# Kernel optimization log

Hardware: AMD Instinct MI355X
Metric: run time of the kernel (lower is better)

Reference implementation:

```python
import jax, jax.numpy as jnp
import numpy as np

N, E, DIN, DOUT = 50000, 625000, 128, 128


def setup_inputs() -> dict:
    key = jax.random.key(0)
    k = jax.random.split(key, 4)
    x = jax.random.normal(k[0], (N, DIN), dtype=jnp.float32)
    edge_index = jax.random.randint(k[1], (2, E), 0, N, dtype=jnp.int32)
    s = 1.0 / np.sqrt(DIN)  # Glorot-ish init like torch Linear
    W_fwd = jax.random.uniform(k[2], (DIN, DOUT), jnp.float32, -s, s)
    W_bwd = jax.random.uniform(k[3], (DIN, DOUT), jnp.float32, -s, s)
    b_fwd = jnp.zeros((DOUT,), jnp.float32)
    b_bwd = jnp.zeros((DOUT,), jnp.float32)
    return {"x": x, "edge_index": edge_index, "W_fwd": W_fwd, "b_fwd": b_fwd,
            "W_bwd": W_bwd, "b_bwd": b_bwd}


def gcn_conv(x, W, b, src, dst, n):
    """PyG GCNConv: add self-loops, symmetric degree norm, gather-scatter aggregate."""
    loops = jnp.arange(n, dtype=src.dtype)
    src2 = jnp.concatenate([src, loops])  # [E+N]
    dst2 = jnp.concatenate([dst, loops])
    ones = jnp.ones(src2.shape[0], dtype=x.dtype)
    deg = jax.ops.segment_sum(ones, dst2, num_segments=n)  # in-degree incl. self-loop
    dinv = jnp.where(deg > 0, jax.lax.rsqrt(deg), 0.0)
    norm = dinv[src2] * dinv[dst2]  # [E+N]
    h = x @ W  # [N, DOUT] dense GEMM before message passing
    msgs = h[src2] * norm[:, None]  # gather + scale, [E+N, DOUT]
    out = jax.ops.segment_sum(msgs, dst2, num_segments=n)  # scatter-add
    return out + b


def reference(x, edge_index, W_fwd, b_fwd, W_bwd, b_bwd):
    src, dst = edge_index[0], edge_index[1]
    n = x.shape[0]
    x_forward = gcn_conv(x, W_fwd, b_fwd, src, dst, n)
    # reversed edge direction for the backward diffusion conv
    x_backward = gcn_conv(x, W_bwd, b_bwd, dst, src, n)
    # dropout omitted (eval mode / deterministic reference)
    return jax.nn.relu(x_forward + x_backward)
```

## Files before the change

### kernel.cpp

```cpp
#include <hip/hip_runtime.h>
#include <hip/hip_bf16.h>
#include <cstdint>

static constexpr int BLK      = 256;
static constexpr int CAP      = 40;
static constexpr int BINSHIFT = 8;
static constexpr int BINNODES = 1 << BINSHIFT;
static constexpr int BINCAP   = BINNODES * CAP / 2;
static constexpr int EPB      = 2048;
static constexpr int OVMAX    = 1024;
static constexpr int NB2MAX   = 512;

typedef __attribute__((ext_vector_type(8))) short bf16x8;
typedef __attribute__((ext_vector_type(4))) float f32x4;

__device__ __forceinline__ float bf16lo(uint32_t u) { return __uint_as_float(u << 16); }
__device__ __forceinline__ float bf16hi(uint32_t u) { return __uint_as_float(u & 0xffff0000u); }
__device__ __forceinline__ float bf16f(unsigned short u) { return __uint_as_float((uint32_t)u << 16); }
__device__ __forceinline__ unsigned short f2bf(float f) {
    __hip_bfloat16 h = __float2bfloat16(f);
    return *(unsigned short*)&h;
}

__global__ __launch_bounds__(BLK) void k_bin_conv(
        const int* __restrict__ src, const int* __restrict__ dst, int ne,
        uint32_t* __restrict__ pair, int* __restrict__ gcnt,
        int* __restrict__ ovcnt, int* __restrict__ ovlist, int nbins, int gbin,
        const float* __restrict__ x, uint32_t* __restrict__ xb32, int nxw, int gxc,
        const float* __restrict__ Wf, const float* __restrict__ Wb,
        unsigned short* __restrict__ WTf, unsigned short* __restrict__ WTb) {
    const int bid = blockIdx.x, tid = threadIdx.x;
    if (bid < gbin) {
        __shared__ uint32_t stage[EPB * 2];
        __shared__ unsigned short binof[EPB * 2];
        __shared__ int hist[NB2MAX];
        __shared__ int lofs[NB2MAX];
        __shared__ int gbase[NB2MAX];
        __shared__ int chunk[NB2MAX / 8];
        const int nb2 = 2 * nbins;
        for (int i = tid; i < nb2; i += BLK) hist[i] = 0;
        __syncthreads();

        int s[8], d[8];
        const int e0 = bid * EPB + tid;
#pragma unroll
        for (int k = 0; k < 8; ++k) {
            int e = e0 + k * BLK;
            bool v = e < ne;
            s[k] = v ? src[e] : -1;
            d[k] = v ? dst[e] : -1;
            if (v) {
                atomicAdd(&hist[d[k] >> BINSHIFT], 1);
                atomicAdd(&hist[nbins + (s[k] >> BINSHIFT)], 1);
            }
        }
        __syncthreads();

        const int nch = (nb2 + 7) >> 3;
        if (tid < nch) {
            int a = 0, base = tid << 3;
#pragma unroll
            for (int k = 0; k < 8; ++k) { int idx = base + k; if (idx < nb2) a += hist[idx]; }
            chunk[tid] = a;
        }
        __syncthreads();
        if (tid == 0) { int a = 0; for (int c = 0; c < nch; ++c) { int t = chunk[c]; chunk[c] = a; a += t; } }
        __syncthreads();
        for (int i = tid; i < nb2; i += BLK) {
            int a = chunk[i >> 3];
            for (int k = (i >> 3) << 3; k < i; ++k) a += hist[k];
            lofs[i] = a;
        }
        __syncthreads();
        for (int i = tid; i < nb2; i += BLK) {
            int c = hist[i];
            gbase[i] = c ? atomicAdd(&gcnt[i], c) : 0;
            hist[i] = lofs[i];
        }
        __syncthreads();
#pragma unroll
        for (int k = 0; k < 8; ++k) {
            if (s[k] >= 0) {
                int b0 = d[k] >> BINSHIFT;
                int p0 = atomicAdd(&hist[b0], 1);
                stage[p0] = ((uint32_t)d[k] << 16) | (uint32_t)s[k];
                binof[p0] = (unsigned short)b0;
                int b1 = nbins + (s[k] >> BINSHIFT);
                int p1 = atomicAdd(&hist[b1], 1);
                stage[p1] = ((uint32_t)s[k] << 16) | (uint32_t)d[k];
                binof[p1] = (unsigned short)b1;
            }
        }
        __syncthreads();
        int nval = ne - bid * EPB; if (nval > EPB) nval = EPB; if (nval < 0) nval = 0;
        const int total = 2 * nval;
        for (int i = tid; i < total; i += BLK) {
            int b = binof[i];
            int gidx = gbase[b] + (i - lofs[b]);
            if (gidx < BINCAP)
                pair[(size_t)b * BINCAP + gidx] = stage[i];
            else {
                int node = (int)(stage[i] >> 16);
                int q = atomicAdd(ovcnt, 1);
                if (q < OVMAX) ovlist[q] = (node << 1) | (b >= nbins ? 1 : 0);
            }
        }
        return;
    }
    if (bid < gbin + gxc) {
        int base = (bid - gbin) * 2048;
        int end = base + 2048; if (end > nxw) end = nxw;
        for (int i = base + tid; i < end; i += BLK) {
            float2 v = ((const float2*)x)[i];
            xb32[i] = ((uint32_t)f2bf(v.y) << 16) | (uint32_t)f2bf(v.x);
        }
        return;
    }
    int wb = bid - gbin - gxc;
    for (int idx = wb * 2048 + tid; idx < (wb + 1) * 2048; idx += BLK) {
        int c = idx >> 7, k = idx & 127;
        WTf[c * 128 + k] = f2bf(Wf[k * 128 + c]);
        WTb[c * 128 + k] = f2bf(Wb[k * 128 + c]);
    }
}

__global__ __launch_bounds__(BLK) void k_build(
        uint32_t* __restrict__ pair, const int* __restrict__ gcnt,
        int* __restrict__ cnt_f, int* __restrict__ cnt_b,
        float* __restrict__ dinv_f, float* __restrict__ dinv_b,
        int* __restrict__ ovcnt, int* __restrict__ ovlist,
        int n, int nbins) {
    const int bid = blockIdx.x, tid = threadIdx.x;
    __shared__ unsigned short buck[BINNODES * CAP];
    __shared__ int lcnt[BINNODES];
    lcnt[tid] = 0;
    __syncthreads();
    int count = gcnt[bid]; if (count > BINCAP) count = BINCAP;
    const uint32_t* pb = pair + (size_t)bid * BINCAP;
    const int dir = bid >= nbins ? 1 : 0;
    for (int i = tid; i < count; i += BLK) {
        uint32_t p = pb[i];
        int l = (p >> 16) & (BINNODES - 1);
        int r = atomicAdd(&lcnt[l], 1);
        if (r < CAP) buck[l * CAP + r] = (unsigned short)(p & 0xffffu);
        else {
            int q = atomicAdd(ovcnt, 1);
            if (q < OVMAX)
                ovlist[q] = (((((bid - dir * nbins) << BINSHIFT) + l)) << 1) | dir;
        }
    }
    __syncthreads();
    const int node = ((bid - dir * nbins) << BINSHIFT) + tid;
    if (node < n) {
        int c = lcnt[tid];
        if (dir) { cnt_b[node] = c; dinv_b[node] = rsqrtf(1.0f + (float)c); }
        else     { cnt_f[node] = c; dinv_f[node] = rsqrtf(1.0f + (float)c); }
    }
    uint32_t* seg = pair + (size_t)bid * BINCAP;
    const uint32_t* b32 = (const uint32_t*)buck;
    for (int i = tid; i < BINCAP; i += BLK) seg[i] = b32[i];
}

__device__ __forceinline__ void accum_range(
        int j0, int j1, int ofs, float sc,
        const uint32_t* __restrict__ xb, int lane, float& a0, float& a1) {
    int j = j0;
    for (; j + 8 <= j1; j += 8) {
        int   o0 = __shfl(ofs, j + 0), o1 = __shfl(ofs, j + 1);
        int   o2 = __shfl(ofs, j + 2), o3 = __shfl(ofs, j + 3);
        int   o4 = __shfl(ofs, j + 4), o5 = __shfl(ofs, j + 5);
        int   o6 = __shfl(ofs, j + 6), o7 = __shfl(ofs, j + 7);
        float s0 = __shfl(sc, j + 0), s1 = __shfl(sc, j + 1);
        float s2 = __shfl(sc, j + 2), s3 = __shfl(sc, j + 3);
        float s4 = __shfl(sc, j + 4), s5 = __shfl(sc, j + 5);
        float s6 = __shfl(sc, j + 6), s7 = __shfl(sc, j + 7);
        uint32_t u0 = xb[(size_t)(o0 + lane)], u1 = xb[(size_t)(o1 + lane)];
        uint32_t u2 = xb[(size_t)(o2 + lane)], u3 = xb[(size_t)(o3 + lane)];
        uint32_t u4 = xb[(size_t)(o4 + lane)], u5 = xb[(size_t)(o5 + lane)];
        uint32_t u6 = xb[(size_t)(o6 + lane)], u7 = xb[(size_t)(o7 + lane)];
        a0 = fmaf(s0, bf16lo(u0), a0); a1 = fmaf(s0, bf16hi(u0), a1);
        a0 = fmaf(s1, bf16lo(u1), a0); a1 = fmaf(s1, bf16hi(u1), a1);
        a0 = fmaf(s2, bf16lo(u2), a0); a1 = fmaf(s2, bf16hi(u2), a1);
        a0 = fmaf(s3, bf16lo(u3), a0); a1 = fmaf(s3, bf16hi(u3), a1);
        a0 = fmaf(s4, bf16lo(u4), a0); a1 = fmaf(s4, bf16hi(u4), a1);
        a0 = fmaf(s5, bf16lo(u5), a0); a1 = fmaf(s5, bf16hi(u5), a1);
        a0 = fmaf(s6, bf16lo(u6), a0); a1 = fmaf(s6, bf16hi(u6), a1);
        a0 = fmaf(s7, bf16lo(u7), a0); a1 = fmaf(s7, bf16hi(u7), a1);
    }
    for (; j + 4 <= j1; j += 4) {
        int   o0 = __shfl(ofs, j + 0), o1 = __shfl(ofs, j + 1);
        int   o2 = __shfl(ofs, j + 2), o3 = __shfl(ofs, j + 3);
        float s0 = __shfl(sc, j + 0), s1 = __shfl(sc, j + 1);
        float s2 = __shfl(sc, j + 2), s3 = __shfl(sc, j + 3);
        uint32_t u0 = xb[(size_t)(o0 + lane)], u1 = xb[(size_t)(o1 + lane)];
        uint32_t u2 = xb[(size_t)(o2 + lane)], u3 = xb[(size_t)(o3 + lane)];
        a0 = fmaf(s0, bf16lo(u0), a0); a1 = fmaf(s0, bf16hi(u0), a1);
        a0 = fmaf(s1, bf16lo(u1), a0); a1 = fmaf(s1, bf16hi(u1), a1);
        a0 = fmaf(s2, bf16lo(u2), a0); a1 = fmaf(s2, bf16hi(u2), a1);
        a0 = fmaf(s3, bf16lo(u3), a0); a1 = fmaf(s3, bf16hi(u3), a1);
    }
    for (; j < j1; ++j) {
        int oj = __shfl(ofs, j); float sj = __shfl(sc, j);
        uint32_t uj = xb[(size_t)(oj + lane)];
        a0 = fmaf(sj, bf16lo(uj), a0); a1 = fmaf(sj, bf16hi(uj), a1);
    }
}

__global__ __launch_bounds__(BLK, 8) void k_gather_gemm(
        const int* __restrict__ cnt_f, const int* __restrict__ cnt_b,
        const unsigned short* __restrict__ adj_f,
        const unsigned short* __restrict__ adj_b,
        const float* __restrict__ dinv_f, const float* __restrict__ dinv_b,
        const uint32_t* __restrict__ xb32,
        const unsigned short* __restrict__ WTf,
        const unsigned short* __restrict__ WTb,
        const float* __restrict__ bfv, const float* __restrict__ bbv,
        float* __restrict__ out, int n, int gnode2,
        const int* __restrict__ ovcnt, const int* __restrict__ ovlist,
        const int* __restrict__ src, const int* __restrict__ dst, int ne) {
    __shared__ __align__(16) char smemU[16 * 528];
    __shared__ int ovflag[16];
    __shared__ int donec;
    __shared__ int lc;
    const int bid = blockIdx.x, tid = threadIdx.x;
    if (bid < gnode2) {
        uint32_t* aggL = (uint32_t*)smemU;
        const int wave = tid >> 6, lane = tid & 63;
        const int node0 = bid * 16;
        if (tid == 0) donec = 0;
        __syncthreads();

        for (int i4 = 0; i4 < 4; ++i4) {
            const int row = wave * 4 + i4;
            const int node = node0 + row;
            int cf = 0, cb = 0;
            bool skip = node >= n;
            if (!skip) { cf = cnt_f[node]; cb = cnt_b[node]; skip = (cf > CAP || cb > CAP); }
            if (lane == 0) ovflag[row] = skip ? 1 : 0;
            if (skip) continue;

            float dvsf = dinv_f[node], dvsb = dinv_b[node];
            uint32_t uv = xb32[(size_t)node * 64 + lane];
            float accf0 = dvsf * dvsf * bf16lo(uv), accf1 = dvsf * dvsf * bf16hi(uv);
            float accb0 = dvsb * dvsb * bf16lo(uv), accb1 = dvsb * dvsb * bf16hi(uv);

            const int mt = cf + cb;
            if (mt <= 64) {
                int ofs = 0; float sc = 0.f;
                if (lane < cf) {
                    int nb = adj_f[node * CAP + lane];
                    ofs = nb * 64;
                    sc  = dvsf * dinv_f[nb];
                } else if (lane < mt) {
                    int nb = adj_b[node * CAP + (lane - cf)];
                    ofs = nb * 64;
                    sc  = dvsb * dinv_b[nb];
                }
                accum_range(0,  cf, ofs, sc, xb32, lane, accf0, accf1);
                accum_range(cf, mt, ofs, sc, xb32, lane, accb0, accb1);
            } else {
                for (int j = 0; j < cf; ++j) {
                    int nb = adj_f[node * CAP + j];
                    float dj = dvsf * dinv_f[nb];
                    uint32_t u = xb32[(size_t)nb * 64 + lane];
                    accf0 = fmaf(dj, bf16lo(u), accf0); accf1 = fmaf(dj, bf16hi(u), accf1);
                }
                for (int j = 0; j < cb; ++j) {
                    int nb = adj_b[node * CAP + j];
                    float dj = dvsb * dinv_b[nb];
                    uint32_t u = xb32[(size_t)nb * 64 + lane];
                    accb0 = fmaf(dj, bf16lo(u), accb0); accb1 = fmaf(dj, bf16hi(u), accb1);
                }
            }
            aggL[row * 132 + lane] =
                ((uint32_t)f2bf(accf1) << 16) | (uint32_t)f2bf(accf0);
            aggL[row * 132 + 64 + lane] =
                ((uint32_t)f2bf(accb1) << 16) | (uint32_t)f2bf(accb0);
        }

        __threadfence_block();
        int prev = 0;
        if (lane == 0) prev = atomicAdd(&donec, 1);
        prev = __shfl(prev, 0);
        if (prev != 3) return;
        __threadfence_block();

        const int q = lane >> 4, t16 = lane & 15;
        const char* arow = smemU + t16 * 528;
        bf16x8 a[8];
#pragma unroll
        for (int s = 0; s < 8; ++s)
            a[s] = *(const bf16x8*)(arow + s * 64 + q * 16);
#pragma unroll
        for (int t = 0; t < 8; ++t) {
            const int col = t * 16 + t16;
            const unsigned short* wrf = WTf + (size_t)col * 128;
            const unsigned short* wrb = WTb + (size_t)col * 128;
            f32x4 c = {0.f, 0.f, 0.f, 0.f};
#pragma unroll
            for (int s = 0; s < 4; ++s)
                c = __builtin_amdgcn_mfma_f32_16x16x32_bf16(
                        a[s], *(const bf16x8*)(wrf + s * 32 + q * 8), c, 0, 0, 0);
#pragma unroll
            for (int s = 0; s < 4; ++s)
                c = __builtin_amdgcn_mfma_f32_16x16x32_bf16(
                        a[4 + s], *(const bf16x8*)(wrb + s * 32 + q * 8), c, 0, 0, 0);
            const float bias = bfv[col] + bbv[col];
#pragma unroll
            for (int r = 0; r < 4; ++r) {
                int row = q * 4 + r;
                int node2 = node0 + row;
                if (node2 < n && !ovflag[row])
                    out[(size_t)node2 * 128 + col] = fmaxf(c[r] + bias, 0.f);
            }
        }
        return;
    }

    int nov = *ovcnt; if (nov > OVMAX) nov = OVMAX;
    if (nov == 0) return;
    int* lst = (int*)smemU;
    float* aggfl = (float*)(smemU);
    __shared__ float afix[256];
    for (int i = bid - gnode2; i < nov; i += 8) {
        int node = ovlist[i] >> 1;
        for (int d2 = 0; d2 < 2; ++d2) {
            const int* key = d2 ? src : dst;
            const int* val = d2 ? dst : src;
            const float* dinv = d2 ? dinv_b : dinv_f;
            float dvs = dinv[node];
            float s0 = 0.f, s1 = 0.f;
            if (tid < 64) {
                uint32_t u = xb32[(size_t)node * 64 + tid];
                s0 = dvs * bf16lo(u); s1 = dvs * bf16hi(u);
            }
            for (int start = 0; start < ne; start += 2048) {
                if (tid == 0) lc = 0;
                __syncthreads();
                int end = min(start + 2048, ne);
                for (int e2 = start + tid; e2 < end; e2 += BLK)
                    if (key[e2] == node) { int qq = atomicAdd(&lc, 1); lst[qq] = val[e2]; }
                __syncthreads();
                int mm = lc;
                if (tid < 64) {
                    for (int j = 0; j < mm; ++j) {
                        int nb = lst[j];
                        float dv = dinv[nb];
                        uint32_t u = xb32[(size_t)nb * 64 + tid];
                        s0 = fmaf(dv, bf16lo(u), s0);
                        s1 = fmaf(dv, bf16hi(u), s1);
                    }
                }
                __syncthreads();
            }
            if (tid < 64) {
                afix[d2 * 128 + 2 * tid]     = bf16f(f2bf(dvs * s0));
                afix[d2 * 128 + 2 * tid + 1] = bf16f(f2bf(dvs * s1));
            }
            __syncthreads();
        }
        if (tid < 128) {
            const int col = tid;
            float acc = bfv[col] + bbv[col];
            const unsigned short* wrf = WTf + (size_t)col * 128;
            const unsigned short* wrb = WTb + (size_t)col * 128;
            for (int k = 0; k < 128; ++k) {
                acc = fmaf(afix[k],       bf16f(wrf[k]), acc);
                acc = fmaf(afix[128 + k], bf16f(wrb[k]), acc);
            }
            out[(size_t)node * 128 + col] = fmaxf(acc, 0.f);
        }
        __syncthreads();
        (void)aggfl;
    }
}

extern "C" void kernel_launch(void* const* d_in, const int* in_sizes, int n_in,
                              void* d_out, int out_size, void* d_ws, size_t ws_size,
                              hipStream_t stream) {
    const float* x  = (const float*)d_in[0];
    const int*   ei = (const int*)d_in[1];
    const float* Wf = (const float*)d_in[2];
    const float* bf = (const float*)d_in[3];
    const float* Wb = (const float*)d_in[4];
    const float* bb = (const float*)d_in[5];

    const int n  = in_sizes[0] / 128;
    const int ne = in_sizes[1] / 2;
    const int* src = ei;
    const int* dst = ei + ne;
    float* out = (float*)d_out;

    const int nbins = (n + BINNODES - 1) >> BINSHIFT;
    const int nb2   = 2 * nbins;

    char* w = (char*)d_ws;
    uint32_t* pair = (uint32_t*)w;              w += (size_t)nb2 * BINCAP * 4;
    uint32_t* xb32 = (uint32_t*)w;              w += (size_t)n * 64 * 4;
    float* dinv_f = (float*)w;                  w += (size_t)n * 4;
    float* dinv_b = (float*)w;                  w += (size_t)n * 4;
    unsigned short* WTf = (unsigned short*)w;   w += 128 * 128 * 2;
    unsigned short* WTb = (unsigned short*)w;   w += 128 * 128 * 2;
    int* cnt_f = (int*)w;                       w += (size_t)n * 4;
    int* cnt_b = (int*)w;                       w += (size_t)n * 4;
    int* gcnt = (int*)w;                        w += (size_t)nb2 * 4;
    int* ovcnt = (int*)w;                       w += 8 * 4;
    int* ovlist = (int*)w;                      w += OVMAX * 4;

    const unsigned short* adj_f = (const unsigned short*)pair;
    const unsigned short* adj_b = adj_f + (size_t)nbins * BINNODES * CAP;

    const int gbin   = (ne + EPB - 1) / EPB;
    const int gxc    = (n * 64 + 2047) / 2048;
    const int gnode2 = (n + 15) / 16;

    hipMemsetAsync(gcnt, 0, (size_t)(nb2 + 8) * 4, stream);

    k_bin_conv<<<gbin + gxc + 8, BLK, 0, stream>>>(src, dst, ne,
                                                   pair, gcnt, ovcnt, ovlist,
                                                   nbins, gbin,
                                                   x, xb32, n * 64, gxc,
                                                   Wf, Wb, WTf, WTb);

    k_build<<<nb2, BLK, 0, stream>>>(pair, gcnt, cnt_f, cnt_b,
                                     dinv_f, dinv_b, ovcnt, ovlist, n, nbins);

    k_gather_gemm<<<gnode2 + 8, BLK, 0, stream>>>(cnt_f, cnt_b, adj_f, adj_b,
                                                  dinv_f, dinv_b, xb32,
                                                  WTf, WTb, bf, bb,
                                                  out, n, gnode2,
                                                  ovcnt, ovlist, src, dst, ne);
}
```

Baseline: 177.4 us.

## Replace global bin atomics with per-block count table; prefetch and split gather-GEMM

The edge binning kernel no longer reserves global slots with atomics. Each block writes its locally sorted pairs contiguously, plus a per-block offset/count table that the build kernel walks to gather each bin, which also removes the memset. The build kernel writes adjacency to a separate zeroed buffer and packs dinv and degree into one 16-byte meta record per node. The gather kernel prefetches the next node's meta, neighbor index, and features, and splits lanes into forward and backward halves of 32. The GEMM stage drops the last-wave-done atomic and uses a block-wide sync so each wave computes a quarter of the columns. This trades fewer global atomics and less serialization for a build pass that loops over every source block per bin with only a small thread count per row.

New measurement: 174.3 us. Within noise of the previous version (-1.7%).

```diff
diff --git a/kernel.cpp b/kernel.cpp
--- a/kernel.cpp
+++ b/kernel.cpp
@@ -6,7 +6,6 @@
 static constexpr int CAP      = 40;
 static constexpr int BINSHIFT = 8;
 static constexpr int BINNODES = 1 << BINSHIFT;
-static constexpr int BINCAP   = BINNODES * CAP / 2;
 static constexpr int EPB      = 2048;
 static constexpr int OVMAX    = 1024;
 static constexpr int NB2MAX   = 512;
@@ -24,18 +23,16 @@
 
 __global__ __launch_bounds__(BLK) void k_bin_conv(
         const int* __restrict__ src, const int* __restrict__ dst, int ne,
-        uint32_t* __restrict__ pair, int* __restrict__ gcnt,
-        int* __restrict__ ovcnt, int* __restrict__ ovlist, int nbins, int gbin,
+        uint32_t* __restrict__ pair, uint32_t* __restrict__ cnttab,
+        int* __restrict__ ovcnt, int nbins, int gbin,
         const float* __restrict__ x, uint32_t* __restrict__ xb32, int nxw, int gxc,
         const float* __restrict__ Wf, const float* __restrict__ Wb,
         unsigned short* __restrict__ WTf, unsigned short* __restrict__ WTb) {
     const int bid = blockIdx.x, tid = threadIdx.x;
     if (bid < gbin) {
         __shared__ uint32_t stage[EPB * 2];
-        __shared__ unsigned short binof[EPB * 2];
         __shared__ int hist[NB2MAX];
         __shared__ int lofs[NB2MAX];
-        __shared__ int gbase[NB2MAX];
         __shared__ int chunk[NB2MAX / 8];
         const int nb2 = 2 * nbins;
         for (int i = tid; i < nb2; i += BLK) hist[i] = 0;
@@ -73,8 +70,8 @@
         }
         __syncthreads();
         for (int i = tid; i < nb2; i += BLK) {
-            int c = hist[i];
-            gbase[i] = c ? atomicAdd(&gcnt[i], c) : 0;
+            cnttab[(size_t)bid * nb2 + i] =
+                ((uint32_t)lofs[i] << 16) | (uint32_t)hist[i];
             hist[i] = lofs[i];
         }
         __syncthreads();
@@ -84,27 +81,17 @@
                 int b0 = d[k] >> BINSHIFT;
                 int p0 = atomicAdd(&hist[b0], 1);
                 stage[p0] = ((uint32_t)d[k] << 16) | (uint32_t)s[k];
-                binof[p0] = (unsigned short)b0;
                 int b1 = nbins + (s[k] >> BINSHIFT);
                 int p1 = atomicAdd(&hist[b1], 1);
                 stage[p1] = ((uint32_t)s[k] << 16) | (uint32_t)d[k];
-                binof[p1] = (unsigned short)b1;
             }
         }
         __syncthreads();
         int nval = ne - bid * EPB; if (nval > EPB) nval = EPB; if (nval < 0) nval = 0;
-        const int total = 2 * nval;
-        for (int i = tid; i < total; i += BLK) {
-            int b = binof[i];
-            int gidx = gbase[b] + (i - lofs[b]);
-            if (gidx < BINCAP)
-                pair[(size_t)b * BINCAP + gidx] = stage[i];
-            else {
-                int node = (int)(stage[i] >> 16);
-                int q = atomicAdd(ovcnt, 1);
-                if (q < OVMAX) ovlist[q] = (node << 1) | (b >= nbins ? 1 : 0);
-            }
-        }
+        const int n4 = (2 * nval + 3) >> 2;
+        uint4* dp = (uint4*)(pair + (size_t)bid * (EPB * 2));
+        const uint4* sp = (const uint4*)stage;
+        for (int i = tid; i < n4; i += BLK) dp[i] = sp[i];
         return;
     }
     if (bid < gbin + gxc) {
@@ -117,6 +104,7 @@
         return;
     }
     int wb = bid - gbin - gxc;
+    if (wb == 0 && tid < 8) ovcnt[tid] = 0;
     for (int idx = wb * 2048 + tid; idx < (wb + 1) * 2048; idx += BLK) {
         int c = idx >> 7, k = idx & 127;
         WTf[c * 128 + k] = f2bf(Wf[k * 128 + c]);
@@ -125,40 +113,52 @@
 }
 
 __global__ __launch_bounds__(BLK) void k_build(
-        uint32_t* __restrict__ pair, const int* __restrict__ gcnt,
-        int* __restrict__ cnt_f, int* __restrict__ cnt_b,
+        const uint32_t* __restrict__ pair, const uint32_t* __restrict__ cnttab,
+        unsigned short* __restrict__ adj,
         float* __restrict__ dinv_f, float* __restrict__ dinv_b,
+        uint4* __restrict__ meta,
         int* __restrict__ ovcnt, int* __restrict__ ovlist,
-        int n, int nbins) {
+        int n, int nbins, int gbin) {
     const int bid = blockIdx.x, tid = threadIdx.x;
+    const int nb2 = 2 * nbins;
     __shared__ unsigned short buck[BINNODES * CAP];
     __shared__ int lcnt[BINNODES];
     lcnt[tid] = 0;
+    for (int i = tid; i < BINNODES * CAP / 2; i += BLK) ((uint32_t*)buck)[i] = 0;
     __syncthreads();
-    int count = gcnt[bid]; if (count > BINCAP) count = BINCAP;
-    const uint32_t* pb = pair + (size_t)bid * BINCAP;
     const int dir = bid >= nbins ? 1 : 0;
-    for (int i = tid; i < count; i += BLK) {
-        uint32_t p = pb[i];
-        int l = (p >> 16) & (BINNODES - 1);
-        int r = atomicAdd(&lcnt[l], 1);
-        if (r < CAP) buck[l * CAP + r] = (unsigned short)(p & 0xffffu);
-        else {
-            int q = atomicAdd(ovcnt, 1);
-            if (q < OVMAX)
-                ovlist[q] = (((((bid - dir * nbins) << BINSHIFT) + l)) << 1) | dir;
+    for (int r = tid; r < gbin; r += BLK) {
+        uint32_t pc = cnttab[(size_t)r * nb2 + bid];
+        int base = (int)(pc >> 16), cnt = (int)(pc & 0xffffu);
+        const uint32_t* pp = pair + (size_t)r * (EPB * 2) + base;
+        for (int j = 0; j < cnt; ++j) {
+            uint32_t p = pp[j];
+            int l = (p >> 16) & (BINNODES - 1);
+            int rk = atomicAdd(&lcnt[l], 1);
+            if (rk < CAP) buck[l * CAP + rk] = (unsigned short)(p & 0xffffu);
+            else {
+                int q = atomicAdd(ovcnt, 1);
+                if (q < OVMAX)
+                    ovlist[q] = (((((bid - dir * nbins) << BINSHIFT) + l)) << 1) | dir;
+            }
         }
     }
     __syncthreads();
     const int node = ((bid - dir * nbins) << BINSHIFT) + tid;
     if (node < n) {
         int c = lcnt[tid];
-        if (dir) { cnt_b[node] = c; dinv_b[node] = rsqrtf(1.0f + (float)c); }
-        else     { cnt_f[node] = c; dinv_f[node] = rsqrtf(1.0f + (float)c); }
-    }
-    uint32_t* seg = pair + (size_t)bid * BINCAP;
+        float dv = rsqrtf(1.0f + (float)c);
+        if (dir) {
+            dinv_b[node] = dv;
+            ((uint2*)&meta[node])[1] = make_uint2(__float_as_uint(dv), (uint32_t)c);
+        } else {
+            dinv_f[node] = dv;
+            ((uint2*)&meta[node])[0] = make_uint2(__float_as_uint(dv), (uint32_t)c);
+        }
+    }
+    uint32_t* seg = (uint32_t*)(adj + (size_t)bid * BINNODES * CAP);
     const uint32_t* b32 = (const uint32_t*)buck;
-    for (int i = tid; i < BINCAP; i += BLK) seg[i] = b32[i];
+    for (int i = tid; i < BINNODES * CAP / 2; i += BLK) seg[i] = b32[i];
 }
 
 __device__ __forceinline__ void accum_range(
@@ -206,8 +206,8 @@
     }
 }
 
-__global__ __launch_bounds__(BLK, 8) void k_gather_gemm(
-        const int* __restrict__ cnt_f, const int* __restrict__ cnt_b,
+__global__ __launch_bounds__(BLK) void k_gather_gemm(
+        const uint4* __restrict__ meta,
         const unsigned short* __restrict__ adj_f,
         const unsigned short* __restrict__ adj_b,
         const float* __restrict__ dinv_f, const float* __restrict__ dinv_b,
@@ -218,57 +218,62 @@
         float* __restrict__ out, int n, int gnode2,
         const int* __restrict__ ovcnt, const int* __restrict__ ovlist,
         const int* __restrict__ src, const int* __restrict__ dst, int ne) {
-    __shared__ __align__(16) char smemU[16 * 528];
+    __shared__ uint32_t aggL[16 * 132];
     __shared__ int ovflag[16];
-    __shared__ int donec;
+    __shared__ int lst[2048];
     __shared__ int lc;
+    __shared__ float afix[256];
     const int bid = blockIdx.x, tid = threadIdx.x;
     if (bid < gnode2) {
-        uint32_t* aggL = (uint32_t*)smemU;
         const int wave = tid >> 6, lane = tid & 63;
+        const int h = lane >> 5, slot = lane & 31;
         const int node0 = bid * 16;
-        if (tid == 0) donec = 0;
-        __syncthreads();
+
+        int np = node0 + wave * 4; if (np >= n) np = n - 1;
+        uint4 mvN = meta[np];
+        int nbN = h ? adj_b[np * CAP + slot] : adj_f[np * CAP + slot];
+        uint32_t uvN = xb32[(size_t)np * 64 + lane];
+        float dnbN = h ? dinv_b[nbN] : dinv_f[nbN];
 
         for (int i4 = 0; i4 < 4; ++i4) {
             const int row = wave * 4 + i4;
             const int node = node0 + row;
-            int cf = 0, cb = 0;
-            bool skip = node >= n;
-            if (!skip) { cf = cnt_f[node]; cb = cnt_b[node]; skip = (cf > CAP || cb > CAP); }
+            uint4 mv = mvN; int nb = nbN; uint32_t uv = uvN; float dnb = dnbN;
+            if (i4 < 3) {
+                int nn = node + 1; if (nn >= n) nn = n - 1;
+                mvN = meta[nn];
+                nbN = h ? adj_b[nn * CAP + slot] : adj_f[nn * CAP + slot];
+                uvN = xb32[(size_t)nn * 64 + lane];
+                dnbN = h ? dinv_b[nbN] : dinv_f[nbN];
+            }
+            float dvsf = __uint_as_float(mv.x), dvsb = __uint_as_float(mv.z);
+            int cf = (int)mv.y, cb = (int)mv.w;
+            bool skip = (node >= n) || (cf > CAP) || (cb > CAP);
             if (lane == 0) ovflag[row] = skip ? 1 : 0;
             if (skip) continue;
 
-            float dvsf = dinv_f[node], dvsb = dinv_b[node];
-            uint32_t uv = xb32[(size_t)node * 64 + lane];
-            float accf0 = dvsf * dvsf * bf16lo(uv), accf1 = dvsf * dvsf * bf16hi(uv);
-            float accb0 = dvsb * dvsb * bf16lo(uv), accb1 = dvsb * dvsb * bf16hi(uv);
-
-            const int mt = cf + cb;
-            if (mt <= 64) {
-                int ofs = 0; float sc = 0.f;
-                if (lane < cf) {
-                    int nb = adj_f[node * CAP + lane];
-                    ofs = nb * 64;
-                    sc  = dvsf * dinv_f[nb];
-                } else if (lane < mt) {
-                    int nb = adj_b[node * CAP + (lane - cf)];
-                    ofs = nb * 64;
-                    sc  = dvsb * dinv_b[nb];
-                }
-                accum_range(0,  cf, ofs, sc, xb32, lane, accf0, accf1);
-                accum_range(cf, mt, ofs, sc, xb32, lane, accb0, accb1);
+            float wf = dvsf * dvsf, wb = dvsb * dvsb;
+            float accf0 = wf * bf16lo(uv), accf1 = wf * bf16hi(uv);
+            float accb0 = wb * bf16lo(uv), accb1 = wb * bf16hi(uv);
+
+            if (cf <= 32 && cb <= 32) {
+                float dvs_h = h ? dvsb : dvsf;
+                int   c_h   = h ? cb : cf;
+                float sc  = (slot < c_h) ? dvs_h * dnb : 0.f;
+                int   ofs = nb * 64;
+                accum_range(0,  cf,      ofs, sc, xb32, lane, accf0, accf1);
+                accum_range(32, 32 + cb, ofs, sc, xb32, lane, accb0, accb1);
             } else {
                 for (int j = 0; j < cf; ++j) {
-                    int nb = adj_f[node * CAP + j];
-                    float dj = dvsf * dinv_f[nb];
-                    uint32_t u = xb32[(size_t)nb * 64 + lane];
+                    int nb2x = adj_f[node * CAP + j];
+                    float dj = dvsf * dinv_f[nb2x];
+                    uint32_t u = xb32[(size_t)nb2x * 64 + lane];
                     accf0 = fmaf(dj, bf16lo(u), accf0); accf1 = fmaf(dj, bf16hi(u), accf1);
                 }
                 for (int j = 0; j < cb; ++j) {
-                    int nb = adj_b[node * CAP + j];
-                    float dj = dvsb * dinv_b[nb];
-                    uint32_t u = xb32[(size_t)nb * 64 + lane];
+                    int nb2x = adj_b[node * CAP + j];
+                    float dj = dvsb * dinv_b[nb2x];
+                    uint32_t u = xb32[(size_t)nb2x * 64 + lane];
                     accb0 = fmaf(dj, bf16lo(u), accb0); accb1 = fmaf(dj, bf16hi(u), accb1);
                 }
             }
@@ -277,23 +282,16 @@
             aggL[row * 132 + 64 + lane] =
                 ((uint32_t)f2bf(accb1) << 16) | (uint32_t)f2bf(accb0);
         }
-
-        __threadfence_block();
-        int prev = 0;
-        if (lane == 0) prev = atomicAdd(&donec, 1);
-        prev = __shfl(prev, 0);
-        if (prev != 3) return;
-        __threadfence_block();
+        __syncthreads();
 
         const int q = lane >> 4, t16 = lane & 15;
-        const char* arow = smemU + t16 * 528;
         bf16x8 a[8];
 #pragma unroll
         for (int s = 0; s < 8; ++s)
-            a[s] = *(const bf16x8*)(arow + s * 64 + q * 16);
-#pragma unroll
-        for (int t = 0; t < 8; ++t) {
-            const int col = t * 16 + t16;
+            a[s] = *(const bf16x8*)((const char*)aggL + t16 * 528 + s * 64 + q * 16);
+#pragma unroll
+        for (int t2 = 0; t2 < 2; ++t2) {
+            const int col = (wave * 2 + t2) * 16 + t16;
             const unsigned short* wrf = WTf + (size_t)col * 128;
             const unsigned short* wrb = WTb + (size_t)col * 128;
             f32x4 c = {0.f, 0.f, 0.f, 0.f};
@@ -319,9 +317,6 @@
 
     int nov = *ovcnt; if (nov > OVMAX) nov = OVMAX;
     if (nov == 0) return;
-    int* lst = (int*)smemU;
-    float* aggfl = (float*)(smemU);
-    __shared__ float afix[256];
     for (int i = bid - gnode2; i < nov; i += 8) {
         int node = ovlist[i] >> 1;
         for (int d2 = 0; d2 < 2; ++d2) {
@@ -371,7 +366,6 @@
             out[(size_t)node * 128 + col] = fmaxf(acc, 0.f);
         }
         __syncthreads();
-        (void)aggfl;
     }
 }
 
@@ -393,39 +387,38 @@
 
     const int nbins = (n + BINNODES - 1) >> BINSHIFT;
     const int nb2   = 2 * nbins;
+    const int gbin  = (ne + EPB - 1) / EPB;
 
     char* w = (char*)d_ws;
-    uint32_t* pair = (uint32_t*)w;              w += (size_t)nb2 * BINCAP * 4;
+    uint32_t* pair = (uint32_t*)w;              w += (size_t)gbin * EPB * 2 * 4;
+    unsigned short* adj = (unsigned short*)w;   w += (size_t)nb2 * BINNODES * CAP * 2;
     uint32_t* xb32 = (uint32_t*)w;              w += (size_t)n * 64 * 4;
+    uint4* meta = (uint4*)w;                    w += (size_t)n * 16;
     float* dinv_f = (float*)w;                  w += (size_t)n * 4;
     float* dinv_b = (float*)w;                  w += (size_t)n * 4;
     unsigned short* WTf = (unsigned short*)w;   w += 128 * 128 * 2;
     unsigned short* WTb = (unsigned short*)w;   w += 128 * 128 * 2;
-    int* cnt_f = (int*)w;                       w += (size_t)n * 4;
-    int* cnt_b = (int*)w;                       w += (size_t)n * 4;
-    int* gcnt = (int*)w;                        w += (size_t)nb2 * 4;
+    uint32_t* cnttab = (uint32_t*)w;            w += (size_t)gbin * nb2 * 4;
     int* ovcnt = (int*)w;                       w += 8 * 4;
     int* ovlist = (int*)w;                      w += OVMAX * 4;
 
-    const unsigned short* adj_f = (const unsigned short*)pair;
-    const unsigned short* adj_b = adj_f + (size_t)nbins * BINNODES * CAP;
-
-    const int gbin   = (ne + EPB - 1) / EPB;
+    const unsigned short* adj_f = adj;
+    const unsigned short* adj_b = adj + (size_t)nbins * BINNODES * CAP;
+
     const int gxc    = (n * 64 + 2047) / 2048;
     const int gnode2 = (n + 15) / 16;
 
-    hipMemsetAsync(gcnt, 0, (size_t)(nb2 + 8) * 4, stream);
-
     k_bin_conv<<<gbin + gxc + 8, BLK, 0, stream>>>(src, dst, ne,
-                                                   pair, gcnt, ovcnt, ovlist,
+                                                   pair, cnttab, ovcnt,
                                                    nbins, gbin,
                                                    x, xb32, n * 64, gxc,
                                                    Wf, Wb, WTf, WTb);
 
-    k_build<<<nb2, BLK, 0, stream>>>(pair, gcnt, cnt_f, cnt_b,
-                                     dinv_f, dinv_b, ovcnt, ovlist, n, nbins);
-
-    k_gather_gemm<<<gnode2 + 8, BLK, 0, stream>>>(cnt_f, cnt_b, adj_f, adj_b,
+    k_build<<<nb2, BLK, 0, stream>>>(pair, cnttab, adj,
+                                     dinv_f, dinv_b, meta,
+                                     ovcnt, ovlist, n, nbins, gbin);
+
+    k_gather_gemm<<<gnode2 + 8, BLK, 0, stream>>>(meta, adj_f, adj_b,
                                                   dinv_f, dinv_b, xb32,
                                                   WTf, WTb, bf, bb,
                                                   out, n, gnode2,
```
